# Optimization experiments

Hardware: AMD Instinct MI355X
Metric: run time of the kernel (lower is better)

## Reference

```python
import jax, jax.numpy as jnp
import numpy as np

EMBED = 256
HEADS = 8
WH, WW = 7, 7
N = WH * WW


def _rel_pos_index(Wh, Ww):
    coords = np.stack(np.meshgrid(np.arange(Wh), np.arange(Ww), indexing='ij'))  # [2,Wh,Ww]
    flat = coords.reshape(2, -1)  # [2, N]
    rel = flat[:, :, None] - flat[:, None, :]  # [2,N,N]
    rel = rel.transpose(1, 2, 0).astype(np.int64)
    rel[:, :, 0] += Wh - 1
    rel[:, :, 1] += Ww - 1
    rel[:, :, 0] *= 2 * Ww - 1
    return rel.sum(-1)  # [N,N]


def setup_inputs() -> dict:
    key = jax.random.key(0)
    ks = jax.random.split(key, 8)
    B = 4096
    nW = 64
    x = jax.random.normal(ks[0], (B, N, EMBED), dtype=jnp.float32)
    mask = jax.random.normal(ks[1], (nW, N, N), dtype=jnp.float32)
    qkv_w = jax.random.normal(ks[2], (3 * EMBED, EMBED), dtype=jnp.float32) * (EMBED ** -0.5)
    qkv_b = jnp.zeros((3 * EMBED,), dtype=jnp.float32)
    proj_w = jax.random.normal(ks[3], (EMBED, EMBED), dtype=jnp.float32) * (EMBED ** -0.5)
    proj_b = jnp.zeros((EMBED,), dtype=jnp.float32)
    bias_table = jax.random.normal(ks[4], ((2 * WH - 1) * (2 * WW - 1), HEADS), dtype=jnp.float32) * 0.02
    return {"x": x, "mask": mask, "qkv_w": qkv_w, "qkv_b": qkv_b,
            "proj_w": proj_w, "proj_b": proj_b, "bias_table": bias_table}


def reference(x, mask, qkv_w, qkv_b, proj_w, proj_b, bias_table):
    B, n, C = x.shape
    hd = C // HEADS
    scale = hd ** -0.5
    rel_idx = jnp.asarray(_rel_pos_index(WH, WW))  # [N,N] int, static
    qkv = (x @ qkv_w.T + qkv_b).reshape(B, n, 3, HEADS, hd)
    qkv = jnp.transpose(qkv, (2, 0, 3, 1, 4))  # [3,B,H,N,hd]
    q, k, v = qkv[0] * scale, qkv[1], qkv[2]
    attn = jnp.einsum('bhqd,bhkd->bhqk', q, k)  # [B,H,N,N]
    rel_bias = bias_table[rel_idx]  # [N,N,H]
    attn = attn + jnp.transpose(rel_bias, (2, 0, 1))[None]
    nW = mask.shape[0]
    attn = attn.reshape(B // nW, nW, HEADS, n, n) + mask[None, :, None]
    attn = attn.reshape(B, HEADS, n, n)
    attn = jax.nn.softmax(attn, axis=-1)
    out = jnp.einsum('bhqk,bhkd->bhqd', attn, v)  # [B,H,N,hd]
    out = jnp.transpose(out, (0, 2, 1, 3)).reshape(B, n, C)
    return out @ proj_w.T + proj_b
```

## Files before the change

kernel.cpp:

```cpp
#include <hip/hip_runtime.h>
#include <hip/hip_bf16.h>

typedef __bf16 bf16x8 __attribute__((ext_vector_type(8)));
typedef float f32x4 __attribute__((ext_vector_type(4)));
typedef short short8 __attribute__((ext_vector_type(8)));
typedef short short4v __attribute__((ext_vector_type(4)));

#define XSTRIDE 264
#define SCRSZ   2304
#define QKSTR   36
#define VSTR    72
#define PSTR    72

#define WS_QW   256u
#define WS_PW   393472u
#define WS_QB   524544u
#define WS_PB   527616u
#define WS_CMB  528640u
#define WS_FULL (528640u + 8388608u)

__device__ __forceinline__ float b2f(short s) {
  unsigned u = ((unsigned)(unsigned short)s) << 16;
  float f; __builtin_memcpy(&f, &u, 4); return f;
}
__device__ __forceinline__ short f2b(float f) {
  unsigned u; __builtin_memcpy(&u, &f, 4);
  u += 0x7FFFu + ((u >> 16) & 1u);
  return (short)(u >> 16);
}
__device__ __forceinline__ bf16x8 ld8(const short* p) {
  short8 s = *(const short8*)p;
  bf16x8 f; __builtin_memcpy(&f, &s, 16); return f;
}
__device__ __forceinline__ float ldE(const void* p, size_t i, int f32) {
  return f32 ? ((const float*)p)[i] : b2f(((const short*)p)[i]);
}
__device__ __forceinline__ f32x4 mfma16(bf16x8 a, bf16x8 b, f32x4 c) {
  return __builtin_amdgcn_mfma_f32_16x16x32_bf16(a, b, c, 0, 0, 0);
}
__device__ __forceinline__ void lgkm0() {
  asm volatile("s_waitcnt lgkmcnt(0)" ::: "memory");
  __builtin_amdgcn_sched_barrier(0);
}

__global__ __launch_bounds__(256) void detect_k(
    const short* p0, int n0, const short* p1, int n1, const short* p2, int n2,
    const short* p3, int n3, const short* p4, int n4, const short* p5, int n5,
    const short* p6, int n6, int* flags)
{
  const short* ps[7] = {p0, p1, p2, p3, p4, p5, p6};
  int ns[7] = {n0, n1, n2, n3, n4, n5, n6};
  int b = blockIdx.x;
  const short* p = ps[b];
  int n = ns[b];
  __shared__ int mx;
  if (threadIdx.x == 0) mx = 0;
  __syncthreads();
  int K = n >> 1; if (K > 4096) K = 4096;
  int lm = 0;
  for (int k = threadIdx.x; k < K; k += 256) {
    int e = (((int)(unsigned short)p[2 * k]) >> 7) & 0xFF;
    lm = lm > e ? lm : e;
  }
  atomicMax(&mx, lm);
  __syncthreads();
  if (threadIdx.x == 0) flags[b] = (mx >= 160) ? 1 : 0;
}

__global__ __launch_bounds__(256) void prep_k(
    const void* __restrict__ qkvw, const void* __restrict__ qkvb,
    const void* __restrict__ projw, const void* __restrict__ projb,
    const void* __restrict__ btab, const void* __restrict__ maskg,
    char* __restrict__ ws, const int* __restrict__ flags, int use_cmb)
{
  const int fm = flags[1], fqw = flags[2], fqb = flags[3];
  const int fpw = flags[4], fpb = flags[5], fbt = flags[6];
  short* qw = (short*)(ws + WS_QW);
  short* pw = (short*)(ws + WS_PW);
  float* qb = (float*)(ws + WS_QB);
  float* pb = (float*)(ws + WS_PB);
  float* cmb = (float*)(ws + WS_CMB);
  const int blk = blockIdx.x, tid = threadIdx.x;
  if (blk < 512) {
    if (!use_cmb) return;
    int widx = blk >> 3, h = blk & 7;
    for (int i = tid; i < 4096; i += 256) {
      int tq = i >> 6, tk = i & 63;
      float v = -1e30f;
      if (tq < 49 && tk < 49) {
        int qr = tq / 7, qc = tq - qr * 7;
        int kr = tk / 7, kc = tk - kr * 7;
        int idx = (qr - kr + 6) * 13 + (qc - kc + 6);
        v = ldE(maskg, (size_t)widx * 2401 + tq * 49 + tk, fm)
          + ldE(btab, (size_t)idx * 8 + h, fbt);
      }
      cmb[(size_t)blk * 4096 + i] = v;
    }
  } else if (blk < 528) {
    int base = (blk - 512) * 12288;
    for (int i = tid; i < 12288; i += 256)
      qw[base + i] = f2b(ldE(qkvw, base + i, fqw));
  } else if (blk < 530) {
    int base = (blk - 528) * 32768;
    for (int i = tid; i < 32768; i += 256)
      pw[base + i] = f2b(ldE(projw, base + i, fpw));
  } else {
    for (int i = tid; i < 768; i += 256) qb[i] = ldE(qkvb, i, fqb);
    if (tid < 256) pb[tid] = ldE(projb, tid, fpb);
  }
}

template<int USE_CMB>
__global__ __launch_bounds__(512, 4) void wmsa(
    const void* __restrict__ xg, const void* __restrict__ maskg,
    const void* __restrict__ btab, const char* __restrict__ ws,
    void* __restrict__ outg, const int* __restrict__ flags)
{
  __shared__ __align__(16) short lds[35328];
  const int tid  = threadIdx.x;
  const int w    = tid >> 6;
  const int lane = tid & 63;
  const int L    = lane & 15;
  const int quad = lane >> 4;
  const int b    = blockIdx.x;

  const int fx = flags[0];
  const int fm = flags[1], fbt = flags[6];

  const short* qw  = (const short*)(ws + WS_QW);
  const short* pw  = (const short*)(ws + WS_PW);
  const float* qb  = (const float*)(ws + WS_QB);
  const float* pb  = (const float*)(ws + WS_PB);
  const float* cmb = (const float*)(ws + WS_CMB);

  short* x_s = lds;
  short* scr = lds + 16896 + w * SCRSZ;

  if (fx) {
    const float* xb = (const float*)xg + (size_t)b * (49 * 256);
    for (int i = tid; i < 1568; i += 512) {
      int t = i >> 5, c8 = i & 31;
      const float* s = xb + t * 256 + c8 * 8;
      f32x4 a = *(const f32x4*)s;
      f32x4 c = *(const f32x4*)(s + 4);
      short8 v;
      v[0] = f2b(a[0]); v[1] = f2b(a[1]); v[2] = f2b(a[2]); v[3] = f2b(a[3]);
      v[4] = f2b(c[0]); v[5] = f2b(c[1]); v[6] = f2b(c[2]); v[7] = f2b(c[3]);
      *(short8*)(x_s + t * XSTRIDE + c8 * 8) = v;
    }
  } else {
    const short* xb = (const short*)xg + (size_t)b * (49 * 256);
    for (int i = tid; i < 1568; i += 512) {
      int t = i >> 5, c8 = i & 31;
      *(short8*)(x_s + t * XSTRIDE + c8 * 8) = *(const short8*)(xb + t * 256 + c8 * 8);
    }
  }
  for (int i = tid; i < 495; i += 512) {
    int t = 49 + i / 33, c8 = i - (i / 33) * 33;
    *(short8*)(x_s + t * XSTRIDE + c8 * 8) = short8{0,0,0,0,0,0,0,0};
  }
  __syncthreads();

  const int h = w;
  const float scale = 0.17677669529663687f;
  bf16x8 fq[4], fk[4], fv[2][2];

  #pragma unroll
  for (int nbo = 0; nbo < 2; nbo++) {
    const int baserow = h * 32 + nbo * 16;
    const short* wr = qw + (size_t)(baserow + L) * 256 + quad * 8;
    bf16x8 wf[8];
    #pragma unroll
    for (int ks = 0; ks < 8; ks++) wf[ks] = ld8(wr + ks * 32);
    const float bias = qb[baserow + L];
    #pragma unroll
    for (int m = 0; m < 4; m++) {
      const short* ar = x_s + (m * 16 + L) * XSTRIDE + quad * 8;
      f32x4 acc = {0.f, 0.f, 0.f, 0.f};
      #pragma unroll
      for (int ks = 0; ks < 8; ks++) acc = mfma16(ld8(ar + ks * 32), wf[ks], acc);
      #pragma unroll
      for (int r = 0; r < 4; r++)
        scr[(m * 16 + quad * 4 + r) * QKSTR + nbo * 16 + L] =
            f2b((acc[r] + bias) * scale);
    }
  }
  lgkm0();
  #pragma unroll
  for (int nbq = 0; nbq < 4; nbq++)
    fq[nbq] = ld8(scr + (nbq * 16 + L) * QKSTR + quad * 8);
  lgkm0();

  #pragma unroll
  for (int nbo = 0; nbo < 2; nbo++) {
    const int baserow = 256 + h * 32 + nbo * 16;
    const short* wr = qw + (size_t)(baserow + L) * 256 + quad * 8;
    bf16x8 wf[8];
    #pragma unroll
    for (int ks = 0; ks < 8; ks++) wf[ks] = ld8(wr + ks * 32);
    const float bias = qb[baserow + L];
    #pragma unroll
    for (int m = 0; m < 4; m++) {
      const short* ar = x_s + (m * 16 + L) * XSTRIDE + quad * 8;
      f32x4 acc = {0.f, 0.f, 0.f, 0.f};
      #pragma unroll
      for (int ks = 0; ks < 8; ks++) acc = mfma16(ld8(ar + ks * 32), wf[ks], acc);
      #pragma unroll
      for (int r = 0; r < 4; r++)
        scr[(m * 16 + quad * 4 + r) * QKSTR + nbo * 16 + L] = f2b(acc[r] + bias);
    }
  }
  lgkm0();
  #pragma unroll
  for (int m = 0; m < 4; m++)
    fk[m] = ld8(scr + (m * 16 + L) * QKSTR + quad * 8);
  lgkm0();

  #pragma unroll
  for (int nbo = 0; nbo < 2; nbo++) {
    const int baserow = 512 + h * 32 + nbo * 16;
    const short* wr = qw + (size_t)(baserow + L) * 256 + quad * 8;
    bf16x8 wf[8];
    #pragma unroll
    for (int ks = 0; ks < 8; ks++) wf[ks] = ld8(wr + ks * 32);
    const float bias = qb[baserow + L];
    #pragma unroll
    for (int m = 0; m < 4; m++) {
      const short* ar = x_s + (m * 16 + L) * XSTRIDE + quad * 8;
      f32x4 acc = {0.f, 0.f, 0.f, 0.f};
      #pragma unroll
      for (int ks = 0; ks < 8; ks++) acc = mfma16(ld8(ar + ks * 32), wf[ks], acc);
      short4v pk;
      #pragma unroll
      for (int r = 0; r < 4; r++) pk[r] = f2b(acc[r] + bias);
      *(short4v*)(scr + (nbo * 16 + L) * VSTR + m * 16 + quad * 4) = pk;
    }
  }
  lgkm0();
  #pragma unroll
  for (int ks2 = 0; ks2 < 2; ks2++)
    #pragma unroll
    for (int blk2 = 0; blk2 < 2; blk2++)
      fv[ks2][blk2] = ld8(scr + (blk2 * 16 + L) * VSTR + ks2 * 32 + quad * 8);
  lgkm0();

  const int widx = b & 63;
  const float* cmbh = cmb + ((size_t)(widx * 8 + h)) * 4096;
  float oacc[4][2][4];
  #pragma unroll
  for (int nbq = 0; nbq < 4; nbq++) {
    const int tq = nbq * 16 + L;
    f32x4 s[4];
    #pragma unroll
    for (int m = 0; m < 4; m++) {
      f32x4 z = {0.f, 0.f, 0.f, 0.f};
      s[m] = mfma16(fk[m], fq[nbq], z);
    }
    float vals[16];
    float mx = -1e30f;
    if (USE_CMB) {
      #pragma unroll
      for (int m = 0; m < 4; m++) {
        f32x4 c4 = *(const f32x4*)(cmbh + tq * 64 + m * 16 + quad * 4);
        #pragma unroll
        for (int r = 0; r < 4; r++) {
          float v = s[m][r] + c4[r];
          vals[m * 4 + r] = v;
          mx = fmaxf(mx, v);
        }
      }
    } else {
      const int tqc = tq < 49 ? tq : 48;
      const int qr = tqc / 7, qc = tqc - qr * 7;
      #pragma unroll
      for (int m = 0; m < 4; m++) {
        #pragma unroll
        for (int r = 0; r < 4; r++) {
          const int tk = m * 16 + quad * 4 + r;
          float v = -1e30f;
          if (tk < 49) {
            const int kr = tk / 7, kc = tk - kr * 7;
            const int idx = (qr - kr + 6) * 13 + (qc - kc + 6);
            v = s[m][r] + ldE(btab, (size_t)idx * 8 + h, fbt)
                        + ldE(maskg, (size_t)widx * 2401 + tqc * 49 + tk, fm);
          }
          vals[m * 4 + r] = v;
          mx = fmaxf(mx, v);
        }
      }
    }
    mx = fmaxf(mx, __shfl_xor(mx, 16));
    mx = fmaxf(mx, __shfl_xor(mx, 32));
    float sum = 0.f;
    #pragma unroll
    for (int i2 = 0; i2 < 16; i2++) { vals[i2] = __expf(vals[i2] - mx); sum += vals[i2]; }
    sum += __shfl_xor(sum, 16);
    sum += __shfl_xor(sum, 32);
    const float inv = 1.f / sum;
    #pragma unroll
    for (int m = 0; m < 4; m++) {
      short4v pk;
      #pragma unroll
      for (int r = 0; r < 4; r++) pk[r] = f2b(vals[m * 4 + r] * inv);
      *(short4v*)(scr + L * PSTR + m * 16 + quad * 4) = pk;
    }
    lgkm0();
    f32x4 o0 = {0.f,0.f,0.f,0.f}, o1 = {0.f,0.f,0.f,0.f};
    #pragma unroll
    for (int ks2 = 0; ks2 < 2; ks2++) {
      bf16x8 fp = ld8(scr + L * PSTR + ks2 * 32 + quad * 8);
      o0 = mfma16(fp, fv[ks2][0], o0);
      o1 = mfma16(fp, fv[ks2][1], o1);
    }
    lgkm0();
    #pragma unroll
    for (int r = 0; r < 4; r++) { oacc[nbq][0][r] = o0[r]; oacc[nbq][1][r] = o1[r]; }
  }

  __syncthreads();
  short* o_s = lds;
  #pragma unroll
  for (int nbq = 0; nbq < 4; nbq++)
    #pragma unroll
    for (int nbd = 0; nbd < 2; nbd++)
      #pragma unroll
      for (int r = 0; r < 4; r++)
        o_s[(nbq * 16 + quad * 4 + r) * XSTRIDE + h * 32 + nbd * 16 + L] =
            f2b(oacc[nbq][nbd][r]);
  __syncthreads();

  {
    const int mb = w & 3, half = w >> 2;
    bf16x8 ao[8];
    const short* orow = o_s + (mb * 16 + L) * XSTRIDE + quad * 8;
    #pragma unroll
    for (int ks = 0; ks < 8; ks++) ao[ks] = ld8(orow + ks * 32);
    for (int i = 0; i < 8; i++) {
      const int nb = half * 8 + i;
      const short* wr = pw + (size_t)(nb * 16 + L) * 256 + quad * 8;
      bf16x8 wf[8];
      #pragma unroll
      for (int ks = 0; ks < 8; ks++) wf[ks] = ld8(wr + ks * 32);
      f32x4 acc = {0.f, 0.f, 0.f, 0.f};
      #pragma unroll
      for (int ks = 0; ks < 8; ks++) acc = mfma16(ao[ks], wf[ks], acc);
      const float bias = pb[nb * 16 + L];
      #pragma unroll
      for (int r = 0; r < 4; r++) {
        const int t = mb * 16 + quad * 4 + r;
        if (t < 49) {
          size_t ofs = (size_t)b * (49 * 256) + (size_t)t * 256 + nb * 16 + L;
          float val = acc[r] + bias;
          if (fx) ((float*)outg)[ofs] = val;
          else    ((short*)outg)[ofs] = f2b(val);
        }
      }
    }
  }
}

extern "C" void kernel_launch(void* const* d_in, const int* in_sizes, int n_in,
                              void* d_out, int out_size, void* d_ws, size_t ws_size,
                              hipStream_t stream) {
  (void)n_in; (void)out_size;
  int B = in_sizes[0] / (49 * 256);
  char* ws = (char*)d_ws;
  int* flags = (int*)ws;
  detect_k<<<7, 256, 0, stream>>>(
      (const short*)d_in[0], in_sizes[0], (const short*)d_in[1], in_sizes[1],
      (const short*)d_in[2], in_sizes[2], (const short*)d_in[3], in_sizes[3],
      (const short*)d_in[4], in_sizes[4], (const short*)d_in[5], in_sizes[5],
      (const short*)d_in[6], in_sizes[6], flags);
  const int use_cmb = ws_size >= (size_t)WS_FULL;
  prep_k<<<531, 256, 0, stream>>>(d_in[2], d_in[3], d_in[4], d_in[5], d_in[6],
                                  d_in[1], ws, flags, use_cmb);
  if (use_cmb)
    wmsa<1><<<B, 512, 0, stream>>>(d_in[0], d_in[1], d_in[6], ws, d_out, flags);
  else
    wmsa<0><<<B, 512, 0, stream>>>(d_in[0], d_in[1], d_in[6], ws, d_out, flags);
}
```

Before: 815.0 us.

## Merge QKV column halves, double-buffer softmax probs, prefetch proj weights

The QK projection now computes both 16-column halves per x-fragment load, so each x fragment is loaded once instead of twice. The Q/K scratch moves to a split-half layout. Softmax probabilities alternate between two LDS buffers, attention outputs go straight into the shared output tile inside the loop (after an added barrier), and the combined-mask loads are hoisted ahead of the QK MFMAs. The output projection double-buffers its weight fragments to hide global load latency. These changes raise register pressure and LDS size, which could reduce occupancy under the 512x4 launch bounds.

```diff
diff --git a/kernel.cpp b/kernel.cpp
--- a/kernel.cpp
+++ b/kernel.cpp
@@ -7,10 +7,12 @@
 typedef short short4v __attribute__((ext_vector_type(4)));
 
 #define XSTRIDE 264
-#define SCRSZ   2304
-#define QKSTR   36
+#define SCRSZ   2560
+#define QKSTR   20
+#define QHALF   1280
 #define VSTR    72
 #define PSTR    72
+#define PBUF    1152
 
 #define WS_QW   256u
 #define WS_PW   393472u
@@ -116,7 +118,7 @@
     const void* __restrict__ btab, const char* __restrict__ ws,
     void* __restrict__ outg, const int* __restrict__ flags)
 {
-  __shared__ __align__(16) short lds[35328];
+  __shared__ __align__(16) short lds[37376];
   const int tid  = threadIdx.x;
   const int w    = tid >> 6;
   const int lane = tid & 63;
@@ -165,55 +167,74 @@
   const float scale = 0.17677669529663687f;
   bf16x8 fq[4], fk[4], fv[2][2];
 
-  #pragma unroll
-  for (int nbo = 0; nbo < 2; nbo++) {
-    const int baserow = h * 32 + nbo * 16;
-    const short* wr = qw + (size_t)(baserow + L) * 256 + quad * 8;
-    bf16x8 wf[8];
-    #pragma unroll
-    for (int ks = 0; ks < 8; ks++) wf[ks] = ld8(wr + ks * 32);
-    const float bias = qb[baserow + L];
+  {
+    const int baserow = h * 32;
+    bf16x8 wf[16];
+    #pragma unroll
+    for (int nbo = 0; nbo < 2; nbo++) {
+      const short* wr = qw + (size_t)(baserow + nbo * 16 + L) * 256 + quad * 8;
+      #pragma unroll
+      for (int ks = 0; ks < 8; ks++) wf[nbo * 8 + ks] = ld8(wr + ks * 32);
+    }
+    const float b0 = qb[baserow + L], b1 = qb[baserow + 16 + L];
     #pragma unroll
     for (int m = 0; m < 4; m++) {
       const short* ar = x_s + (m * 16 + L) * XSTRIDE + quad * 8;
-      f32x4 acc = {0.f, 0.f, 0.f, 0.f};
-      #pragma unroll
-      for (int ks = 0; ks < 8; ks++) acc = mfma16(ld8(ar + ks * 32), wf[ks], acc);
-      #pragma unroll
-      for (int r = 0; r < 4; r++)
-        scr[(m * 16 + quad * 4 + r) * QKSTR + nbo * 16 + L] =
-            f2b((acc[r] + bias) * scale);
+      bf16x8 xf[8];
+      #pragma unroll
+      for (int ks = 0; ks < 8; ks++) xf[ks] = ld8(ar + ks * 32);
+      f32x4 a0 = {0.f,0.f,0.f,0.f}, a1 = {0.f,0.f,0.f,0.f};
+      #pragma unroll
+      for (int ks = 0; ks < 8; ks++) {
+        a0 = mfma16(xf[ks], wf[ks], a0);
+        a1 = mfma16(xf[ks], wf[8 + ks], a1);
+      }
+      #pragma unroll
+      for (int r = 0; r < 4; r++) {
+        scr[(m * 16 + quad * 4 + r) * QKSTR + L]         = f2b((a0[r] + b0) * scale);
+        scr[QHALF + (m * 16 + quad * 4 + r) * QKSTR + L] = f2b((a1[r] + b1) * scale);
+      }
     }
   }
   lgkm0();
   #pragma unroll
   for (int nbq = 0; nbq < 4; nbq++)
-    fq[nbq] = ld8(scr + (nbq * 16 + L) * QKSTR + quad * 8);
-  lgkm0();
-
-  #pragma unroll
-  for (int nbo = 0; nbo < 2; nbo++) {
-    const int baserow = 256 + h * 32 + nbo * 16;
-    const short* wr = qw + (size_t)(baserow + L) * 256 + quad * 8;
-    bf16x8 wf[8];
-    #pragma unroll
-    for (int ks = 0; ks < 8; ks++) wf[ks] = ld8(wr + ks * 32);
-    const float bias = qb[baserow + L];
+    fq[nbq] = ld8(scr + (quad >> 1) * QHALF + (nbq * 16 + L) * QKSTR + (quad & 1) * 8);
+  lgkm0();
+
+  {
+    const int baserow = 256 + h * 32;
+    bf16x8 wf[16];
+    #pragma unroll
+    for (int nbo = 0; nbo < 2; nbo++) {
+      const short* wr = qw + (size_t)(baserow + nbo * 16 + L) * 256 + quad * 8;
+      #pragma unroll
+      for (int ks = 0; ks < 8; ks++) wf[nbo * 8 + ks] = ld8(wr + ks * 32);
+    }
+    const float b0 = qb[baserow + L], b1 = qb[baserow + 16 + L];
     #pragma unroll
     for (int m = 0; m < 4; m++) {
       const short* ar = x_s + (m * 16 + L) * XSTRIDE + quad * 8;
-      f32x4 acc = {0.f, 0.f, 0.f, 0.f};
-      #pragma unroll
-      for (int ks = 0; ks < 8; ks++) acc = mfma16(ld8(ar + ks * 32), wf[ks], acc);
-      #pragma unroll
-      for (int r = 0; r < 4; r++)
-        scr[(m * 16 + quad * 4 + r) * QKSTR + nbo * 16 + L] = f2b(acc[r] + bias);
+      bf16x8 xf[8];
+      #pragma unroll
+      for (int ks = 0; ks < 8; ks++) xf[ks] = ld8(ar + ks * 32);
+      f32x4 a0 = {0.f,0.f,0.f,0.f}, a1 = {0.f,0.f,0.f,0.f};
+      #pragma unroll
+      for (int ks = 0; ks < 8; ks++) {
+        a0 = mfma16(xf[ks], wf[ks], a0);
+        a1 = mfma16(xf[ks], wf[8 + ks], a1);
+      }
+      #pragma unroll
+      for (int r = 0; r < 4; r++) {
+        scr[(m * 16 + quad * 4 + r) * QKSTR + L]         = f2b(a0[r] + b0);
+        scr[QHALF + (m * 16 + quad * 4 + r) * QKSTR + L] = f2b(a1[r] + b1);
+      }
     }
   }
   lgkm0();
   #pragma unroll
   for (int m = 0; m < 4; m++)
-    fk[m] = ld8(scr + (m * 16 + L) * QKSTR + quad * 8);
+    fk[m] = ld8(scr + (quad >> 1) * QHALF + (m * 16 + L) * QKSTR + (quad & 1) * 8);
   lgkm0();
 
   #pragma unroll
@@ -244,12 +265,20 @@
       fv[ks2][blk2] = ld8(scr + (blk2 * 16 + L) * VSTR + ks2 * 32 + quad * 8);
   lgkm0();
 
+  __syncthreads();
+
   const int widx = b & 63;
   const float* cmbh = cmb + ((size_t)(widx * 8 + h)) * 4096;
-  float oacc[4][2][4];
+  short* o_s = lds;
   #pragma unroll
   for (int nbq = 0; nbq < 4; nbq++) {
     const int tq = nbq * 16 + L;
+    f32x4 c4[4];
+    if (USE_CMB) {
+      #pragma unroll
+      for (int m = 0; m < 4; m++)
+        c4[m] = *(const f32x4*)(cmbh + tq * 64 + m * 16 + quad * 4);
+    }
     f32x4 s[4];
     #pragma unroll
     for (int m = 0; m < 4; m++) {
@@ -261,10 +290,9 @@
     if (USE_CMB) {
       #pragma unroll
       for (int m = 0; m < 4; m++) {
-        f32x4 c4 = *(const f32x4*)(cmbh + tq * 64 + m * 16 + quad * 4);
         #pragma unroll
         for (int r = 0; r < 4; r++) {
-          float v = s[m][r] + c4[r];
+          float v = s[m][r] + c4[m][r];
           vals[m * 4 + r] = v;
           mx = fmaxf(mx, v);
         }
@@ -297,36 +325,28 @@
     sum += __shfl_xor(sum, 16);
     sum += __shfl_xor(sum, 32);
     const float inv = 1.f / sum;
+    short* pbuf = scr + (nbq & 1) * PBUF;
     #pragma unroll
     for (int m = 0; m < 4; m++) {
       short4v pk;
       #pragma unroll
       for (int r = 0; r < 4; r++) pk[r] = f2b(vals[m * 4 + r] * inv);
-      *(short4v*)(scr + L * PSTR + m * 16 + quad * 4) = pk;
+      *(short4v*)(pbuf + L * PSTR + m * 16 + quad * 4) = pk;
     }
     lgkm0();
     f32x4 o0 = {0.f,0.f,0.f,0.f}, o1 = {0.f,0.f,0.f,0.f};
     #pragma unroll
     for (int ks2 = 0; ks2 < 2; ks2++) {
-      bf16x8 fp = ld8(scr + L * PSTR + ks2 * 32 + quad * 8);
+      bf16x8 fp = ld8(pbuf + L * PSTR + ks2 * 32 + quad * 8);
       o0 = mfma16(fp, fv[ks2][0], o0);
       o1 = mfma16(fp, fv[ks2][1], o1);
     }
-    lgkm0();
-    #pragma unroll
-    for (int r = 0; r < 4; r++) { oacc[nbq][0][r] = o0[r]; oacc[nbq][1][r] = o1[r]; }
-  }
-
-  __syncthreads();
-  short* o_s = lds;
-  #pragma unroll
-  for (int nbq = 0; nbq < 4; nbq++)
-    #pragma unroll
-    for (int nbd = 0; nbd < 2; nbd++)
-      #pragma unroll
-      for (int r = 0; r < 4; r++)
-        o_s[(nbq * 16 + quad * 4 + r) * XSTRIDE + h * 32 + nbd * 16 + L] =
-            f2b(oacc[nbq][nbd][r]);
+    #pragma unroll
+    for (int r = 0; r < 4; r++) {
+      o_s[(nbq * 16 + quad * 4 + r) * XSTRIDE + h * 32 + L]      = f2b(o0[r]);
+      o_s[(nbq * 16 + quad * 4 + r) * XSTRIDE + h * 32 + 16 + L] = f2b(o1[r]);
+    }
+  }
   __syncthreads();
 
   {
@@ -335,15 +355,23 @@
     const short* orow = o_s + (mb * 16 + L) * XSTRIDE + quad * 8;
     #pragma unroll
     for (int ks = 0; ks < 8; ks++) ao[ks] = ld8(orow + ks * 32);
-    for (int i = 0; i < 8; i++) {
-      const int nb = half * 8 + i;
+    int nb = half * 8;
+    bf16x8 cur[8];
+    {
       const short* wr = pw + (size_t)(nb * 16 + L) * 256 + quad * 8;
-      bf16x8 wf[8];
-      #pragma unroll
-      for (int ks = 0; ks < 8; ks++) wf[ks] = ld8(wr + ks * 32);
+      #pragma unroll
+      for (int ks = 0; ks < 8; ks++) cur[ks] = ld8(wr + ks * 32);
+    }
+    for (int i = 0; i < 8; i++, nb++) {
+      bf16x8 nxt[8];
+      if (i < 7) {
+        const short* wr = pw + (size_t)((nb + 1) * 16 + L) * 256 + quad * 8;
+        #pragma unroll
+        for (int ks = 0; ks < 8; ks++) nxt[ks] = ld8(wr + ks * 32);
+      }
       f32x4 acc = {0.f, 0.f, 0.f, 0.f};
       #pragma unroll
-      for (int ks = 0; ks < 8; ks++) acc = mfma16(ao[ks], wf[ks], acc);
+      for (int ks = 0; ks < 8; ks++) acc = mfma16(ao[ks], cur[ks], acc);
       const float bias = pb[nb * 16 + L];
       #pragma unroll
       for (int r = 0; r < 4; r++) {
@@ -355,6 +383,8 @@
           else    ((short*)outg)[ofs] = f2b(val);
         }
       }
+      #pragma unroll
+      for (int ks = 0; ks < 8; ks++) cur[ks] = nxt[ks];
     }
   }
 }
```

Measured after the change: 824.2 us. Within noise of the previous version (+1.1%).
